# Kernel optimization log

Measured on AMD Instinct MI355X. Metric: run time of the kernel, lower is better.

## Reference

```python
import jax, jax.numpy as jnp
import numpy as np

B, N, F = 16, 1024, 256
HEADS, K, DOUT = 8, 512, 256
TAU = 1.0
EPS = 1e-08


def setup_inputs() -> dict:
    key = jax.random.key(0)
    k1, k2, k3, k4, k5, k6 = jax.random.split(key, 6)
    return {
        'Q': jax.random.normal(k1, (B, N, F), dtype=jnp.float32),
        'keys': jax.random.uniform(k2, (HEADS, K, F), dtype=jnp.float32),
        'conv_w': jax.random.normal(k3, (HEADS,), dtype=jnp.float32),
        'lin_w': jax.random.normal(k4, (DOUT, F), dtype=jnp.float32) * 0.05,
        'lin_b': jax.random.normal(k5, (DOUT,), dtype=jnp.float32) * 0.05,
        'mask': jax.random.randint(k6, (B, N), 0, 2, dtype=jnp.int32),
    }


def kl_reg(C):
    # C: (B, N, K)
    P = C ** 2
    cn = jnp.sum(C, axis=-2, keepdims=True) + EPS          # sum over N
    P = P / cn
    pn = jnp.sum(P, axis=-1, keepdims=True) + EPS          # sum over K
    P = P / pn
    kl = jnp.sum(P * (jnp.log(P + EPS) - jnp.log(C + EPS)))
    return 100.0 * kl


def memconv_fwd(Q, keys, conv_w, lin_w, lin_b, fmask):
    # pairwise L2 distance Q (B,N,F) vs keys (H,K,F) -> C (B,H,N,K)
    q2 = jnp.sum(Q * Q, axis=-1)                            # (B,N)
    k2 = jnp.sum(keys * keys, axis=-1)                      # (H,K)
    qk = jnp.einsum('bnf,hkf->bhnk', Q, keys)               # (B,H,N,K)
    d2 = q2[:, None, :, None] + k2[None, :, None, :] - 2.0 * qk
    C = jnp.sqrt(jnp.maximum(d2, 0.0))
    em = fmask[:, None, :, None]                            # (B,1,N,1) broadcast
    C = C * em
    # student-t kernel (gmn variant)
    C = (1.0 + C ** 2 / TAU) ** (-(0.5 * TAU + 0.5))
    C = C / jnp.sum(C, axis=-1, keepdims=True)
    C = C * em
    # conv1x1 over heads -> (B,N,K)
    C = jnp.einsum('bhnk,h->bnk', C, conv_w)
    C = jax.nn.softmax(C, axis=-1)
    C = C * fmask[:, :, None]
    kl = kl_reg(C)
    V = jnp.einsum('bnk,bnf->bkf', C, Q)                    # (B,K,F)
    out = jax.nn.leaky_relu(jnp.einsum('bkf,of->bko', V, lin_w) + lin_b, 0.01)
    return out, kl


def reference(Q, keys, conv_w, lin_w, lin_b, mask):
    fmask = mask.astype(Q.dtype)
    return memconv_fwd(Q, keys, conv_w, lin_w, lin_b, fmask)
```

## Files before the change

### kernel.cpp

```cpp
#include <hip/hip_runtime.h>
#include <math.h>

#define Bc 16
#define Nc 1024
#define Fc 256
#define Hc 8
#define Kc 512
#define DOUTc 256
#define EPSc 1e-8f

typedef short v8s __attribute__((ext_vector_type(8)));
typedef float v4f __attribute__((ext_vector_type(4)));

__device__ __forceinline__ float waveReduceSum(float v) {
    v += __shfl_xor(v, 32); v += __shfl_xor(v, 16); v += __shfl_xor(v, 8);
    v += __shfl_xor(v, 4);  v += __shfl_xor(v, 2);  v += __shfl_xor(v, 1);
    return v;
}

__device__ __forceinline__ unsigned short f2bf(float f) {
    unsigned int u = __float_as_uint(f);
    u = (u + 0x7fffu + ((u >> 16) & 1u)) >> 16;
    return (unsigned short)u;
}

__global__ __launch_bounds__(256) void prep_all(
    const float* __restrict__ Q, const float* __restrict__ keys,
    const float* __restrict__ lin_w,
    unsigned short* __restrict__ Qb, float* __restrict__ q2g,
    float* __restrict__ k2g, unsigned short* __restrict__ Kp,
    unsigned short* __restrict__ Qbp, unsigned short* __restrict__ Wp,
    float* __restrict__ cn, float* __restrict__ klout) {
    __shared__ unsigned short T2[32][66];
    const int bx = blockIdx.x;
    const int tid = threadIdx.x;
    if (bx < 4096) {
        int row = bx * 4 + (tid >> 6);
        int l = tid & 63;
        float4 v = *(const float4*)(Q + (size_t)row * Fc + l * 4);
        float s = v.x * v.x + v.y * v.y + v.z * v.z + v.w * v.w;
        *(ushort4*)(Qb + (size_t)row * Fc + l * 4) =
            make_ushort4(f2bf(v.x), f2bf(v.y), f2bf(v.z), f2bf(v.w));
        s = waveReduceSum(s);
        if (l == 0) q2g[row] = s;
    } else if (bx < 5120) {
        int row = (bx - 4096) * 4 + (tid >> 6);
        int l = tid & 63;
        float4 v = *(const float4*)(keys + (size_t)row * Fc + l * 4);
        float s = v.x * v.x + v.y * v.y + v.z * v.z + v.w * v.w;
        s = waveReduceSum(s);
        if (l == 0) k2g[row] = s;
    } else if (bx < 5632) {
        int t = (bx - 5120) * 256 + tid;
        int lane = t & 63, ci = t >> 6;
        int ct = ci & 7, ks = (ci >> 3) & 7, wv = (ci >> 6) & 3, h = ci >> 8;
        int qd = lane >> 4, li = lane & 15;
        int col = h * 512 + wv * 128 + ct * 16 + li;
        const float* src = keys + (size_t)col * Fc + ks * 32 + qd * 8;
        float4 a = *(const float4*)src;
        float4 b = *(const float4*)(src + 4);
        *(ushort4*)(Kp + (size_t)t * 8) = make_ushort4(f2bf(a.x), f2bf(a.y), f2bf(a.z), f2bf(a.w));
        *(ushort4*)(Kp + (size_t)t * 8 + 4) = make_ushort4(f2bf(b.x), f2bf(b.y), f2bf(b.z), f2bf(b.w));
    } else if (bx < 7680) {
        int i = bx - 5632;
        int n0 = (i & 31) * 32, f0 = ((i >> 5) & 3) * 64, bb = i >> 7;
        {
            int n_l = tid >> 3, f_l = (tid & 7) * 8;
            const float* src = Q + ((size_t)(bb * Nc + n0 + n_l)) * Fc + f0 + f_l;
            float4 a = *(const float4*)src;
            float4 b = *(const float4*)(src + 4);
            T2[n_l][f_l + 0] = f2bf(a.x); T2[n_l][f_l + 1] = f2bf(a.y);
            T2[n_l][f_l + 2] = f2bf(a.z); T2[n_l][f_l + 3] = f2bf(a.w);
            T2[n_l][f_l + 4] = f2bf(b.x); T2[n_l][f_l + 5] = f2bf(b.y);
            T2[n_l][f_l + 6] = f2bf(b.z); T2[n_l][f_l + 7] = f2bf(b.w);
        }
        __syncthreads();
        int c = tid >> 6, L = tid & 63;
        int qd = L >> 4, li = L & 15;
        unsigned short o[8];
#pragma unroll
        for (int j = 0; j < 8; j++) o[j] = T2[qd * 8 + j][c * 16 + li];
        size_t idx = ((((size_t)bb * 16 + (f0 >> 4) + c) * 32 + (n0 >> 5)) * 64 + L) * 8;
        *(ushort4*)(Qbp + idx) = make_ushort4(o[0], o[1], o[2], o[3]);
        *(ushort4*)(Qbp + idx + 4) = make_ushort4(o[4], o[5], o[6], o[7]);
    } else if (bx < 7712) {
        int t = (bx - 7680) * 256 + tid;
        int lane = t & 63, ci = t >> 6;
        int ot = ci >> 3, fs = ci & 7;
        int qd = lane >> 4, li = lane & 15;
        const float* src = lin_w + (size_t)(ot * 16 + li) * Fc + fs * 32 + qd * 8;
        float4 a = *(const float4*)src;
        float4 b = *(const float4*)(src + 4);
        *(ushort4*)(Wp + (size_t)t * 8) = make_ushort4(f2bf(a.x), f2bf(a.y), f2bf(a.z), f2bf(a.w));
        *(ushort4*)(Wp + (size_t)t * 8 + 4) = make_ushort4(f2bf(b.x), f2bf(b.y), f2bf(b.z), f2bf(b.w));
    } else {
        int i = (bx - 7712) * 256 + tid;
        float4 z = make_float4(0.f, 0.f, 0.f, 0.f);
        float4* d = (float4*)(cn + (size_t)i * 16);
        d[0] = z; d[1] = z; d[2] = z; d[3] = z;
        if (bx == 7712 && tid == 0) *klout = 0.f;
    }
}

__global__ __launch_bounds__(256, 1) void cmfma_kernel(
    const unsigned short* __restrict__ Qb, const unsigned short* __restrict__ Kp,
    const float* __restrict__ q2g, const float* __restrict__ k2g,
    const float* __restrict__ conv_w, const int* __restrict__ mask,
    float* __restrict__ C, float* __restrict__ cn,
    unsigned short* __restrict__ Ctp) {
    __shared__ float redbuf[4][32];
    __shared__ short Tb[512][36];
    const int tid = threadIdx.x;
    const int wv = tid >> 6, L = tid & 63;
    const int qd = L >> 4, li = L & 15;
    const int gr0 = blockIdx.x * 32;
    const int b = gr0 >> 10;

    float q2r[2][4], mrow[2][4];
#pragma unroll
    for (int s = 0; s < 2; s++)
#pragma unroll
        for (int r = 0; r < 4; r++) {
            int gr = gr0 + s * 16 + qd * 4 + r;
            q2r[s][r] = q2g[gr];
            mrow[s][r] = (float)mask[gr];
        }

    v8s A[2][8];
#pragma unroll
    for (int s = 0; s < 2; s++) {
        const unsigned short* qa = Qb + (size_t)(gr0 + s * 16 + li) * Fc + qd * 8;
#pragma unroll
        for (int ks = 0; ks < 8; ks++) A[s][ks] = *(const v8s*)(qa + ks * 32);
    }

    v4f D[2][8], S[2][8];
#pragma unroll
    for (int s = 0; s < 2; s++)
#pragma unroll
        for (int ct = 0; ct < 8; ct++) {
            D[s][ct] = (v4f){0.f, 0.f, 0.f, 0.f};
            S[s][ct] = (v4f){0.f, 0.f, 0.f, 0.f};
        }

    const unsigned short* kwbase = Kp + (size_t)L * 8;
    v8s Bc0[8], Bn[8];
    {
        const unsigned short* p0 = kwbase + (size_t)(wv * 64) * 512;
#pragma unroll
        for (int ct = 0; ct < 8; ct++) Bc0[ct] = *(const v8s*)(p0 + ct * 512);
    }

#define KSTEP(kk, CUR, NXT)                                                        \
    do {                                                                           \
        int hn = h * 8 + (kk) + 1;                                                 \
        int hh = (hn >> 3) & 7, kn = hn & 7;                                       \
        const unsigned short* pb =                                                 \
            kwbase + (size_t)(((hh * 4 + wv) * 64 + kn * 8)) * 512;                \
        _Pragma("unroll") for (int ct = 0; ct < 8; ct++)                           \
            NXT[ct] = *(const v8s*)(pb + ct * 512);                                \
        _Pragma("unroll") for (int ct = 0; ct < 8; ct++)                           \
            D[0][ct] = __builtin_amdgcn_mfma_f32_16x16x32_bf16(A[0][kk], CUR[ct],  \
                                                               D[0][ct], 0, 0, 0);\
        _Pragma("unroll") for (int ct = 0; ct < 8; ct++)                           \
            D[1][ct] = __builtin_amdgcn_mfma_f32_16x16x32_bf16(A[1][kk], CUR[ct],  \
                                                               D[1][ct], 0, 0, 0);\
    } while (0)

    for (int h = 0; h < Hc; ++h) {
        float wh = conv_w[h];
        KSTEP(0, Bc0, Bn); KSTEP(1, Bn, Bc0);
        KSTEP(2, Bc0, Bn); KSTEP(3, Bn, Bc0);
        KSTEP(4, Bc0, Bn); KSTEP(5, Bn, Bc0);
        KSTEP(6, Bc0, Bn); KSTEP(7, Bn, Bc0);

        float rs[2][4] = {{0.f, 0.f, 0.f, 0.f}, {0.f, 0.f, 0.f, 0.f}};
#pragma unroll
        for (int ct = 0; ct < 8; ct++) {
            float k2v = k2g[h * Kc + wv * 128 + ct * 16 + li];
#pragma unroll
            for (int s = 0; s < 2; s++)
#pragma unroll
                for (int r = 0; r < 4; r++) {
                    float d2 = fmaxf(q2r[s][r] + k2v - 2.f * D[s][ct][r], 0.f) * mrow[s][r];
                    float t = __builtin_amdgcn_rcpf(1.f + d2);
                    D[s][ct][r] = t;
                    rs[s][r] += t;
                }
        }
#pragma unroll
        for (int s = 0; s < 2; s++)
#pragma unroll
            for (int r = 0; r < 4; r++) {
                rs[s][r] += __shfl_xor(rs[s][r], 1, 16);
                rs[s][r] += __shfl_xor(rs[s][r], 2, 16);
                rs[s][r] += __shfl_xor(rs[s][r], 4, 16);
                rs[s][r] += __shfl_xor(rs[s][r], 8, 16);
            }
        if (li == 0) {
#pragma unroll
            for (int s = 0; s < 2; s++)
#pragma unroll
                for (int r = 0; r < 4; r++) redbuf[wv][s * 16 + qd * 4 + r] = rs[s][r];
        }
        __syncthreads();
        float sc[2][4];
#pragma unroll
        for (int s = 0; s < 2; s++)
#pragma unroll
            for (int r = 0; r < 4; r++) {
                int rw = s * 16 + qd * 4 + r;
                float tot = redbuf[0][rw] + redbuf[1][rw] + redbuf[2][rw] + redbuf[3][rw];
                sc[s][r] = wh * __builtin_amdgcn_rcpf(tot);
            }
        __syncthreads();
#pragma unroll
        for (int s = 0; s < 2; s++)
#pragma unroll
            for (int ct = 0; ct < 8; ct++)
#pragma unroll
                for (int r = 0; r < 4; r++) {
                    S[s][ct][r] += sc[s][r] * D[s][ct][r];
                    D[s][ct][r] = 0.f;
                }
    }
#undef KSTEP

    float mx[2][4] = {{-1e30f, -1e30f, -1e30f, -1e30f}, {-1e30f, -1e30f, -1e30f, -1e30f}};
#pragma unroll
    for (int s = 0; s < 2; s++)
#pragma unroll
        for (int ct = 0; ct < 8; ct++)
#pragma unroll
            for (int r = 0; r < 4; r++) mx[s][r] = fmaxf(mx[s][r], S[s][ct][r]);
#pragma unroll
    for (int s = 0; s < 2; s++)
#pragma unroll
        for (int r = 0; r < 4; r++) {
            mx[s][r] = fmaxf(mx[s][r], __shfl_xor(mx[s][r], 1, 16));
            mx[s][r] = fmaxf(mx[s][r], __shfl_xor(mx[s][r], 2, 16));
            mx[s][r] = fmaxf(mx[s][r], __shfl_xor(mx[s][r], 4, 16));
            mx[s][r] = fmaxf(mx[s][r], __shfl_xor(mx[s][r], 8, 16));
        }
    if (li == 0) {
#pragma unroll
        for (int s = 0; s < 2; s++)
#pragma unroll
            for (int r = 0; r < 4; r++) redbuf[wv][s * 16 + qd * 4 + r] = mx[s][r];
    }
    __syncthreads();
#pragma unroll
    for (int s = 0; s < 2; s++)
#pragma unroll
        for (int r = 0; r < 4; r++) {
            int rw = s * 16 + qd * 4 + r;
            mx[s][r] = fmaxf(fmaxf(redbuf[0][rw], redbuf[1][rw]),
                             fmaxf(redbuf[2][rw], redbuf[3][rw]));
        }
    __syncthreads();
    float es[2][4] = {{0.f, 0.f, 0.f, 0.f}, {0.f, 0.f, 0.f, 0.f}};
#pragma unroll
    for (int s = 0; s < 2; s++)
#pragma unroll
        for (int ct = 0; ct < 8; ct++)
#pragma unroll
            for (int r = 0; r < 4; r++) {
                float e = __expf(S[s][ct][r] - mx[s][r]);
                S[s][ct][r] = e;
                es[s][r] += e;
            }
#pragma unroll
    for (int s = 0; s < 2; s++)
#pragma unroll
        for (int r = 0; r < 4; r++) {
            es[s][r] += __shfl_xor(es[s][r], 1, 16);
            es[s][r] += __shfl_xor(es[s][r], 2, 16);
            es[s][r] += __shfl_xor(es[s][r], 4, 16);
            es[s][r] += __shfl_xor(es[s][r], 8, 16);
        }
    if (li == 0) {
#pragma unroll
        for (int s = 0; s < 2; s++)
#pragma unroll
            for (int r = 0; r < 4; r++) redbuf[wv][s * 16 + qd * 4 + r] = es[s][r];
    }
    __syncthreads();
    float inv[2][4];
#pragma unroll
    for (int s = 0; s < 2; s++)
#pragma unroll
        for (int r = 0; r < 4; r++) {
            int rw = s * 16 + qd * 4 + r;
            float tot = redbuf[0][rw] + redbuf[1][rw] + redbuf[2][rw] + redbuf[3][rw];
            inv[s][r] = mrow[s][r] / tot;
        }
#pragma unroll
    for (int ct = 0; ct < 8; ct++) {
        int k = wv * 128 + ct * 16 + li;
        float colsum = 0.f;
#pragma unroll
        for (int s = 0; s < 2; s++) {
            float cv[4];
#pragma unroll
            for (int r = 0; r < 4; r++) {
                cv[r] = S[s][ct][r] * inv[s][r];
                C[(size_t)(gr0 + s * 16 + qd * 4 + r) * Kc + k] = cv[r];
                colsum += cv[r];
            }
            short4 t4;
            t4.x = (short)f2bf(cv[0]); t4.y = (short)f2bf(cv[1]);
            t4.z = (short)f2bf(cv[2]); t4.w = (short)f2bf(cv[3]);
            *(short4*)&Tb[k][s * 16 + qd * 4] = t4;
        }
        colsum += __shfl_xor(colsum, 16);
        colsum += __shfl_xor(colsum, 32);
        if (qd == 0) atomicAdd(&cn[b * Kc + k], colsum);
    }
    __syncthreads();
    {
        const int ns0 = (gr0 & 1023) >> 5;
#pragma unroll
        for (int kk = 0; kk < 2; kk++) {
            int k = tid * 2 + kk;
            int kt = k >> 4, klo = k & 15;
            size_t cbase = (((size_t)b * 32 + kt) * 32 + ns0) * 512;
#pragma unroll
            for (int q2i = 0; q2i < 4; q2i++) {
                short4 lo = *(short4*)&Tb[k][q2i * 8];
                short4 hi = *(short4*)&Tb[k][q2i * 8 + 4];
                short4* d = (short4*)(Ctp + cbase + (size_t)(q2i * 16 + klo) * 8);
                d[0] = lo; d[1] = hi;
            }
        }
    }
}

__global__ __launch_bounds__(256) void vmfma_kernel(
    const unsigned short* __restrict__ Ctp, const unsigned short* __restrict__ Qbp,
    unsigned short* __restrict__ Vp) {
    __shared__ short Vt[64][76];
    int tid = threadIdx.x;
    int bx = blockIdx.x;
    int w = tid >> 6, L = tid & 63;
    int qd = L >> 4, li = L & 15;
    int wr = w >> 1, wc = w & 1;
    int bb = bx >> 5;
    int rem = bx & 31;
    int ktb = rem >> 2, ftb = rem & 3;
    int KT0 = ktb * 4 + wr * 2;
    int FT0 = ftb * 4 + wc * 2;
    const unsigned short* pa0 = Ctp + (((size_t)bb * 32 + KT0) * 32) * 512 + L * 8;
    const unsigned short* pa1 = pa0 + (size_t)32 * 512;
    const unsigned short* pb0 = Qbp + (((size_t)bb * 16 + FT0) * 32) * 512 + L * 8;
    const unsigned short* pb1 = pb0 + (size_t)32 * 512;
    v4f acc[2][2];
#pragma unroll
    for (int a = 0; a < 2; a++)
#pragma unroll
        for (int c = 0; c < 2; c++) acc[a][c] = (v4f){0.f, 0.f, 0.f, 0.f};

    v8s A0 = *(const v8s*)pa0, A1 = *(const v8s*)pa1;
    v8s B0 = *(const v8s*)pb0, B1 = *(const v8s*)pb1;
    for (int ns = 0; ns < 32; ns++) {
        int nsn = (ns + 1) & 31;
        v8s A0n = *(const v8s*)(pa0 + nsn * 512);
        v8s A1n = *(const v8s*)(pa1 + nsn * 512);
        v8s B0n = *(const v8s*)(pb0 + nsn * 512);
        v8s B1n = *(const v8s*)(pb1 + nsn * 512);
        acc[0][0] = __builtin_amdgcn_mfma_f32_16x16x32_bf16(A0, B0, acc[0][0], 0, 0, 0);
        acc[0][1] = __builtin_amdgcn_mfma_f32_16x16x32_bf16(A0, B1, acc[0][1], 0, 0, 0);
        acc[1][0] = __builtin_amdgcn_mfma_f32_16x16x32_bf16(A1, B0, acc[1][0], 0, 0, 0);
        acc[1][1] = __builtin_amdgcn_mfma_f32_16x16x32_bf16(A1, B1, acc[1][1], 0, 0, 0);
        A0 = A0n; A1 = A1n; B0 = B0n; B1 = B1n;
    }
#pragma unroll
    for (int a = 0; a < 2; a++)
#pragma unroll
        for (int c = 0; c < 2; c++)
#pragma unroll
            for (int r = 0; r < 4; r++)
                Vt[(wr * 2 + a) * 16 + qd * 4 + r][(wc * 2 + c) * 16 + li] =
                    (short)f2bf(acc[a][c][r]);
    __syncthreads();
    {
        int ci = tid >> 5, s5 = tid & 31;
        int mtl = ci >> 1, fsl = ci & 1;
        size_t mt_g = (size_t)bb * 32 + ktb * 4 + mtl;
        size_t fs_g = (size_t)ftb * 2 + fsl;
#pragma unroll
        for (int half = 0; half < 2; half++) {
            int L2 = s5 + half * 32;
            int qd2 = L2 >> 4, li2 = L2 & 15;
            short4 x0 = *(short4*)&Vt[mtl * 16 + li2][fsl * 32 + qd2 * 8];
            short4 x1 = *(short4*)&Vt[mtl * 16 + li2][fsl * 32 + qd2 * 8 + 4];
            short4* d = (short4*)(Vp + ((mt_g * 8 + fs_g) * 64 + L2) * 8);
            d[0] = x0; d[1] = x1;
        }
    }
}

__global__ __launch_bounds__(256) void ofma_kl_kernel(
    const unsigned short* __restrict__ Vp, const unsigned short* __restrict__ Wp,
    const float* __restrict__ bias, float* __restrict__ out,
    const float* __restrict__ C, const float* __restrict__ cn,
    float* __restrict__ klout) {
    __shared__ float red[4];
    int tid = threadIdx.x;
    int bx = blockIdx.x;
    if (bx < 512) {
        int w = tid >> 6, L = tid & 63;
        int qd = L >> 4, li = L & 15;
        int wr = w >> 1, wc = w & 1;
        int mtb = bx & 127, otb = bx >> 7;
        int MT0 = mtb * 4 + wr * 2;
        int OT0 = otb * 4 + wc * 2;
        const unsigned short* pa0 = Vp + ((size_t)MT0 * 8) * 512 + L * 8;
        const unsigned short* pa1 = pa0 + (size_t)8 * 512;
        const unsigned short* pb0 = Wp + ((size_t)OT0 * 8) * 512 + L * 8;
        const unsigned short* pb1 = pb0 + (size_t)8 * 512;
        v4f acc[2][2];
#pragma unroll
        for (int a = 0; a < 2; a++)
#pragma unroll
            for (int c = 0; c < 2; c++) acc[a][c] = (v4f){0.f, 0.f, 0.f, 0.f};
#pragma unroll
        for (int fs = 0; fs < 8; fs++) {
            v8s A0 = *(const v8s*)(pa0 + fs * 512);
            v8s A1 = *(const v8s*)(pa1 + fs * 512);
            v8s B0 = *(const v8s*)(pb0 + fs * 512);
            v8s B1 = *(const v8s*)(pb1 + fs * 512);
            acc[0][0] = __builtin_amdgcn_mfma_f32_16x16x32_bf16(A0, B0, acc[0][0], 0, 0, 0);
            acc[0][1] = __builtin_amdgcn_mfma_f32_16x16x32_bf16(A0, B1, acc[0][1], 0, 0, 0);
            acc[1][0] = __builtin_amdgcn_mfma_f32_16x16x32_bf16(A1, B0, acc[1][0], 0, 0, 0);
            acc[1][1] = __builtin_amdgcn_mfma_f32_16x16x32_bf16(A1, B1, acc[1][1], 0, 0, 0);
        }
#pragma unroll
        for (int c = 0; c < 2; c++) {
            float bv = bias[(OT0 + c) * 16 + li];
#pragma unroll
            for (int a = 0; a < 2; a++)
#pragma unroll
                for (int r = 0; r < 4; r++) {
                    int m = (MT0 + a) * 16 + qd * 4 + r;
                    int o = (OT0 + c) * 16 + li;
                    float x = acc[a][c][r] + bv;
                    out[(size_t)m * DOUTc + o] = x > 0.f ? x : 0.01f * x;
                }
        }
    } else {
        int bk = bx - 512;
        int w = tid >> 6, l = tid & 63;
        float kacc = 0.f;
#pragma unroll
        for (int rr = 0; rr < 4; rr++) {
            int row = bk * 16 + w * 4 + rr;
            int b = row >> 10;
            const float* cp = C + (size_t)row * Kc + l * 8;
            const float* np = cn + b * Kc + l * 8;
            float4 c0 = *(const float4*)cp;
            float4 c1 = *(const float4*)(cp + 4);
            float4 n0 = *(const float4*)np;
            float4 n1 = *(const float4*)(np + 4);
            float p[8];
            p[0] = c0.x * c0.x / (n0.x + EPSc); p[1] = c0.y * c0.y / (n0.y + EPSc);
            p[2] = c0.z * c0.z / (n0.z + EPSc); p[3] = c0.w * c0.w / (n0.w + EPSc);
            p[4] = c1.x * c1.x / (n1.x + EPSc); p[5] = c1.y * c1.y / (n1.y + EPSc);
            p[6] = c1.z * c1.z / (n1.z + EPSc); p[7] = c1.w * c1.w / (n1.w + EPSc);
            float s = p[0] + p[1] + p[2] + p[3] + p[4] + p[5] + p[6] + p[7];
            float pn = waveReduceSum(s) + EPSc;
            float rpn = 1.0f / pn;
            float cc[8] = {c0.x, c0.y, c0.z, c0.w, c1.x, c1.y, c1.z, c1.w};
#pragma unroll
            for (int j = 0; j < 8; j++) {
                float P = p[j] * rpn;
                kacc += P * __logf((P + EPSc) / (cc[j] + EPSc));
            }
        }
        kacc = waveReduceSum(kacc);
        if (l == 0) red[w] = kacc;
        __syncthreads();
        if (tid == 0)
            atomicAdd(klout, 100.f * (red[0] + red[1] + red[2] + red[3]));
    }
}

extern "C" void kernel_launch(void* const* d_in, const int* in_sizes, int n_in,
                              void* d_out, int out_size, void* d_ws, size_t ws_size,
                              hipStream_t stream) {
    const float* Q = (const float*)d_in[0];
    const float* keys = (const float*)d_in[1];
    const float* conv_w = (const float*)d_in[2];
    const float* lin_w = (const float*)d_in[3];
    const float* lin_b = (const float*)d_in[4];
    const int* mask = (const int*)d_in[5];

    float* out = (float*)d_out;
    float* kl = out + (size_t)Bc * Kc * DOUTc;

    float* ws = (float*)d_ws;
    float* C = ws;
    float* k2 = C + (size_t)Bc * Nc * Kc;
    float* cn = k2 + (size_t)Hc * Kc;
    float* q2 = cn + (size_t)Bc * Kc;
    unsigned short* Qb = (unsigned short*)(q2 + (size_t)Bc * Nc);
    unsigned short* Kp = Qb + (size_t)Bc * Nc * Fc;
    unsigned short* Ctp = Kp + (size_t)Hc * Kc * Fc;
    unsigned short* Qbp = Ctp + (size_t)Bc * Nc * Kc;
    unsigned short* Vp = Qbp + (size_t)Bc * Nc * Fc;
    unsigned short* Wp = Vp + (size_t)Bc * Kc * Fc;

    prep_all<<<7714, 256, 0, stream>>>(Q, keys, lin_w, Qb, q2, k2, Kp, Qbp, Wp, cn, kl);
    cmfma_kernel<<<Bc * Nc / 32, 256, 0, stream>>>(Qb, Kp, q2, k2, conv_w, mask, C, cn, Ctp);
    vmfma_kernel<<<512, 256, 0, stream>>>(Ctp, Qbp, Vp);
    ofma_kl_kernel<<<1536, 256, 0, stream>>>(Vp, Wp, lin_b, out, C, cn, kl);
}
```

Before: 200.5 us.

## Fuse V aggregation and output linear into one kernel via LDS

Merges the C^T·Q matmul and the output linear+leaky-relu into a single kernel: each block computes a full 16x256 V tile, stages it in LDS as bf16, and immediately multiplies by the packed weights. This removes the Vp global buffer write/read and one kernel launch, and lets the output GEMM overlap with the KL blocks in the same grid. In exchange each block rereads the whole Q slice per batch, increasing Q traffic (mostly L2), and the retiling changes per-wave register use.

```diff
diff --git a/kernel.cpp b/kernel.cpp
--- a/kernel.cpp
+++ b/kernel.cpp
@@ -335,117 +335,70 @@
     }
 }
 
-__global__ __launch_bounds__(256) void vmfma_kernel(
+__global__ __launch_bounds__(256) void vout_kl_kernel(
     const unsigned short* __restrict__ Ctp, const unsigned short* __restrict__ Qbp,
-    unsigned short* __restrict__ Vp) {
-    __shared__ short Vt[64][76];
-    int tid = threadIdx.x;
-    int bx = blockIdx.x;
-    int w = tid >> 6, L = tid & 63;
-    int qd = L >> 4, li = L & 15;
-    int wr = w >> 1, wc = w & 1;
-    int bb = bx >> 5;
-    int rem = bx & 31;
-    int ktb = rem >> 2, ftb = rem & 3;
-    int KT0 = ktb * 4 + wr * 2;
-    int FT0 = ftb * 4 + wc * 2;
-    const unsigned short* pa0 = Ctp + (((size_t)bb * 32 + KT0) * 32) * 512 + L * 8;
-    const unsigned short* pa1 = pa0 + (size_t)32 * 512;
-    const unsigned short* pb0 = Qbp + (((size_t)bb * 16 + FT0) * 32) * 512 + L * 8;
-    const unsigned short* pb1 = pb0 + (size_t)32 * 512;
-    v4f acc[2][2];
-#pragma unroll
-    for (int a = 0; a < 2; a++)
-#pragma unroll
-        for (int c = 0; c < 2; c++) acc[a][c] = (v4f){0.f, 0.f, 0.f, 0.f};
-
-    v8s A0 = *(const v8s*)pa0, A1 = *(const v8s*)pa1;
-    v8s B0 = *(const v8s*)pb0, B1 = *(const v8s*)pb1;
-    for (int ns = 0; ns < 32; ns++) {
-        int nsn = (ns + 1) & 31;
-        v8s A0n = *(const v8s*)(pa0 + nsn * 512);
-        v8s A1n = *(const v8s*)(pa1 + nsn * 512);
-        v8s B0n = *(const v8s*)(pb0 + nsn * 512);
-        v8s B1n = *(const v8s*)(pb1 + nsn * 512);
-        acc[0][0] = __builtin_amdgcn_mfma_f32_16x16x32_bf16(A0, B0, acc[0][0], 0, 0, 0);
-        acc[0][1] = __builtin_amdgcn_mfma_f32_16x16x32_bf16(A0, B1, acc[0][1], 0, 0, 0);
-        acc[1][0] = __builtin_amdgcn_mfma_f32_16x16x32_bf16(A1, B0, acc[1][0], 0, 0, 0);
-        acc[1][1] = __builtin_amdgcn_mfma_f32_16x16x32_bf16(A1, B1, acc[1][1], 0, 0, 0);
-        A0 = A0n; A1 = A1n; B0 = B0n; B1 = B1n;
-    }
-#pragma unroll
-    for (int a = 0; a < 2; a++)
-#pragma unroll
-        for (int c = 0; c < 2; c++)
-#pragma unroll
-            for (int r = 0; r < 4; r++)
-                Vt[(wr * 2 + a) * 16 + qd * 4 + r][(wc * 2 + c) * 16 + li] =
-                    (short)f2bf(acc[a][c][r]);
-    __syncthreads();
-    {
-        int ci = tid >> 5, s5 = tid & 31;
-        int mtl = ci >> 1, fsl = ci & 1;
-        size_t mt_g = (size_t)bb * 32 + ktb * 4 + mtl;
-        size_t fs_g = (size_t)ftb * 2 + fsl;
-#pragma unroll
-        for (int half = 0; half < 2; half++) {
-            int L2 = s5 + half * 32;
-            int qd2 = L2 >> 4, li2 = L2 & 15;
-            short4 x0 = *(short4*)&Vt[mtl * 16 + li2][fsl * 32 + qd2 * 8];
-            short4 x1 = *(short4*)&Vt[mtl * 16 + li2][fsl * 32 + qd2 * 8 + 4];
-            short4* d = (short4*)(Vp + ((mt_g * 8 + fs_g) * 64 + L2) * 8);
-            d[0] = x0; d[1] = x1;
-        }
-    }
-}
-
-__global__ __launch_bounds__(256) void ofma_kl_kernel(
-    const unsigned short* __restrict__ Vp, const unsigned short* __restrict__ Wp,
-    const float* __restrict__ bias, float* __restrict__ out,
-    const float* __restrict__ C, const float* __restrict__ cn,
-    float* __restrict__ klout) {
+    const unsigned short* __restrict__ Wp, const float* __restrict__ bias,
+    float* __restrict__ out, const float* __restrict__ C,
+    const float* __restrict__ cn, float* __restrict__ klout) {
+    __shared__ short Vt[16][264];
     __shared__ float red[4];
     int tid = threadIdx.x;
     int bx = blockIdx.x;
     if (bx < 512) {
         int w = tid >> 6, L = tid & 63;
         int qd = L >> 4, li = L & 15;
-        int wr = w >> 1, wc = w & 1;
-        int mtb = bx & 127, otb = bx >> 7;
-        int MT0 = mtb * 4 + wr * 2;
-        int OT0 = otb * 4 + wc * 2;
-        const unsigned short* pa0 = Vp + ((size_t)MT0 * 8) * 512 + L * 8;
-        const unsigned short* pa1 = pa0 + (size_t)8 * 512;
-        const unsigned short* pb0 = Wp + ((size_t)OT0 * 8) * 512 + L * 8;
-        const unsigned short* pb1 = pb0 + (size_t)8 * 512;
-        v4f acc[2][2];
-#pragma unroll
-        for (int a = 0; a < 2; a++)
-#pragma unroll
-            for (int c = 0; c < 2; c++) acc[a][c] = (v4f){0.f, 0.f, 0.f, 0.f};
+        int bb = bx >> 5, kt = bx & 31;
+        const unsigned short* pa = Ctp + (((size_t)bb * 32 + kt) * 32) * 512 + L * 8;
+        const unsigned short* pbb = Qbp + (((size_t)bb * 16 + w * 4) * 32) * 512 + L * 8;
+        v4f acc[4];
+#pragma unroll
+        for (int c = 0; c < 4; c++) acc[c] = (v4f){0.f, 0.f, 0.f, 0.f};
+        v8s Ac = *(const v8s*)pa;
+        v8s Bv[4];
+#pragma unroll
+        for (int c = 0; c < 4; c++) Bv[c] = *(const v8s*)(pbb + (size_t)(c * 32) * 512);
+        for (int ns = 0; ns < 32; ns++) {
+            int nsn = (ns + 1) & 31;
+            v8s An = *(const v8s*)(pa + (size_t)nsn * 512);
+            v8s Bn[4];
+#pragma unroll
+            for (int c = 0; c < 4; c++)
+                Bn[c] = *(const v8s*)(pbb + (size_t)(c * 32 + nsn) * 512);
+#pragma unroll
+            for (int c = 0; c < 4; c++)
+                acc[c] = __builtin_amdgcn_mfma_f32_16x16x32_bf16(Ac, Bv[c], acc[c], 0, 0, 0);
+            Ac = An;
+#pragma unroll
+            for (int c = 0; c < 4; c++) Bv[c] = Bn[c];
+        }
+#pragma unroll
+        for (int c = 0; c < 4; c++)
+#pragma unroll
+            for (int r = 0; r < 4; r++)
+                Vt[qd * 4 + r][(w * 4 + c) * 16 + li] = (short)f2bf(acc[c][r]);
+        __syncthreads();
+        v4f o2[4];
+#pragma unroll
+        for (int c = 0; c < 4; c++) o2[c] = (v4f){0.f, 0.f, 0.f, 0.f};
+        const unsigned short* pw = Wp + ((size_t)(w * 4) * 8) * 512 + L * 8;
 #pragma unroll
         for (int fs = 0; fs < 8; fs++) {
-            v8s A0 = *(const v8s*)(pa0 + fs * 512);
-            v8s A1 = *(const v8s*)(pa1 + fs * 512);
-            v8s B0 = *(const v8s*)(pb0 + fs * 512);
-            v8s B1 = *(const v8s*)(pb1 + fs * 512);
-            acc[0][0] = __builtin_amdgcn_mfma_f32_16x16x32_bf16(A0, B0, acc[0][0], 0, 0, 0);
-            acc[0][1] = __builtin_amdgcn_mfma_f32_16x16x32_bf16(A0, B1, acc[0][1], 0, 0, 0);
-            acc[1][0] = __builtin_amdgcn_mfma_f32_16x16x32_bf16(A1, B0, acc[1][0], 0, 0, 0);
-            acc[1][1] = __builtin_amdgcn_mfma_f32_16x16x32_bf16(A1, B1, acc[1][1], 0, 0, 0);
-        }
-#pragma unroll
-        for (int c = 0; c < 2; c++) {
-            float bv = bias[(OT0 + c) * 16 + li];
-#pragma unroll
-            for (int a = 0; a < 2; a++)
-#pragma unroll
-                for (int r = 0; r < 4; r++) {
-                    int m = (MT0 + a) * 16 + qd * 4 + r;
-                    int o = (OT0 + c) * 16 + li;
-                    float x = acc[a][c][r] + bv;
-                    out[(size_t)m * DOUTc + o] = x > 0.f ? x : 0.01f * x;
-                }
+            v8s Af = *(const v8s*)&Vt[li][fs * 32 + qd * 8];
+#pragma unroll
+            for (int c = 0; c < 4; c++) {
+                v8s Bw = *(const v8s*)(pw + (size_t)(c * 8 + fs) * 512);
+                o2[c] = __builtin_amdgcn_mfma_f32_16x16x32_bf16(Af, Bw, o2[c], 0, 0, 0);
+            }
+        }
+#pragma unroll
+        for (int c = 0; c < 4; c++) {
+            float bv = bias[(w * 4 + c) * 16 + li];
+#pragma unroll
+            for (int r = 0; r < 4; r++) {
+                float x = o2[c][r] + bv;
+                out[((size_t)bb * 512 + kt * 16 + qd * 4 + r) * DOUTc + (w * 4 + c) * 16 + li] =
+                    x > 0.f ? x : 0.01f * x;
+            }
         }
     } else {
         int bk = bx - 512;
@@ -506,11 +459,9 @@
     unsigned short* Kp = Qb + (size_t)Bc * Nc * Fc;
     unsigned short* Ctp = Kp + (size_t)Hc * Kc * Fc;
     unsigned short* Qbp = Ctp + (size_t)Bc * Nc * Kc;
-    unsigned short* Vp = Qbp + (size_t)Bc * Nc * Fc;
-    unsigned short* Wp = Vp + (size_t)Bc * Kc * Fc;
+    unsigned short* Wp = Qbp + (size_t)Bc * Nc * Fc;
 
     prep_all<<<7714, 256, 0, stream>>>(Q, keys, lin_w, Qb, q2, k2, Kp, Qbp, Wp, cn, kl);
     cmfma_kernel<<<Bc * Nc / 32, 256, 0, stream>>>(Qb, Kp, q2, k2, conv_w, mask, C, cn, Ctp);
-    vmfma_kernel<<<512, 256, 0, stream>>>(Ctp, Qbp, Vp);
-    ofma_kl_kernel<<<1536, 256, 0, stream>>>(Vp, Wp, lin_b, out, C, cn, kl);
-}
+    vout_kl_kernel<<<1536, 256, 0, stream>>>(Ctp, Qbp, Wp, lin_b, out, C, cn, kl);
+}
```

Result: faster. 192.9 us (-3.8%).
